# Performance work log

Measured on AMD Instinct MI355X. Metric: run time of the kernel, lower is better.

## Reference

```python
import jax, jax.numpy as jnp
import numpy as np

EMBED_DIM = 1024
NUM_HEADS = 16
HEAD_DIM = EMBED_DIM // NUM_HEADS


def setup_inputs() -> dict:
    key = jax.random.key(0)
    k1, k2, k3, k4, k5 = jax.random.split(key, 5)
    B, T, C = 4, 2048, EMBED_DIM
    scale = 1.0 / np.sqrt(C)
    return {
        "x": jax.random.normal(k1, (B, T, C), dtype=jnp.float32),
        "W_qkv": jax.random.normal(k2, (3 * C, C), dtype=jnp.float32) * scale,
        "b_qkv": jax.random.normal(k3, (3 * C,), dtype=jnp.float32) * 0.02,
        "W_proj": jax.random.normal(k4, (C, C), dtype=jnp.float32) * scale,
        "b_proj": jax.random.normal(k5, (C,), dtype=jnp.float32) * 0.02,
    }


def reference(x, W_qkv, b_qkv, W_proj, b_proj):
    B, T, C = x.shape
    H, D = NUM_HEADS, HEAD_DIM
    qkv = x @ W_qkv.T + b_qkv                      # [B,T,3C]
    q, k, v = jnp.split(qkv, 3, axis=-1)
    q = q.reshape(B, T, H, D).transpose(0, 2, 1, 3)  # [B,H,T,D]
    k = k.reshape(B, T, H, D).transpose(0, 2, 1, 3)
    v = v.reshape(B, T, H, D).transpose(0, 2, 1, 3)
    scores = jnp.einsum("bhqd,bhkd->bhqk", q, k) / np.sqrt(D)  # [B,H,T,T]
    causal = jnp.tril(jnp.ones((T, T), dtype=bool))
    scores = jnp.where(causal, scores, -jnp.inf)
    attn = jax.nn.softmax(scores, axis=-1)
    out = jnp.einsum("bhqk,bhkd->bhqd", attn, v)   # [B,H,T,D]
    out = out.transpose(0, 2, 1, 3).reshape(B, T, C)
    return out @ W_proj.T + b_proj
```

## Files before the change

### kernel.cpp

```cpp
#include <hip/hip_runtime.h>
#include <math.h>

#define EMBED 1024
#define NHEAD 16
#define HDIM  64
#define SEQT  2048
#define BATCH 4

typedef __bf16 bf16x4 __attribute__((ext_vector_type(4)));
typedef __bf16 bf16x8 __attribute__((ext_vector_type(8)));
typedef float  f32x4  __attribute__((ext_vector_type(4)));

#define AS1 __attribute__((address_space(1)))
#define AS3 __attribute__((address_space(3)))
#define GLD_LDS16(gp, lp) __builtin_amdgcn_global_load_lds( \
    (const AS1 unsigned int*)(gp), (AS3 unsigned int*)(lp), 16, 0, 0)

#define QSCALE 0.180336880f

__device__ __forceinline__ unsigned short f2bf_hw(float f) {
    union { __bf16 h; unsigned short u; } c; c.h = (__bf16)f; return c.u;
}

__global__ __launch_bounds__(256)
void cvt_all(const float* __restrict__ x, const float* __restrict__ wq,
             const float* __restrict__ wp,
             unsigned short* __restrict__ xb, unsigned short* __restrict__ wqb,
             unsigned short* __restrict__ wpb)
{
    const int N1 = 2097152;
    const int N2 = 786432;
    int i = blockIdx.x * 256 + threadIdx.x;
    const float4* src; ushort4* dst; int j;
    if (i < N1)            { src = (const float4*)x;  dst = (ushort4*)xb;  j = i; }
    else if (i < N1 + N2)  { src = (const float4*)wq; dst = (ushort4*)wqb; j = i - N1; }
    else                   { src = (const float4*)wp; dst = (ushort4*)wpb; j = i - N1 - N2; }
    float4 v = src[j];
    ushort4 o;
    o.x = f2bf_hw(v.x); o.y = f2bf_hw(v.y); o.z = f2bf_hw(v.z); o.w = f2bf_hw(v.w);
    dst[j] = o;
}

template<int MODE>
__global__ __launch_bounds__(256)
void gemm_bt_mfma(const unsigned short* __restrict__ A, const unsigned short* __restrict__ Bw,
                  const float* __restrict__ bias,
                  void* out0, void* out1, void* out2,
                  int M, int N, int K)
{
    __shared__ __align__(16) unsigned short Asm[2][128 * 32];
    __shared__ __align__(16) unsigned short Bsm[2][128 * 32];

    const int tid  = threadIdx.x;
    const int lane = tid & 63;
    const int wave = tid >> 6;
    const int wm = wave >> 1, wn = wave & 1;
    const int col = lane & 15, quad = lane >> 4;
    const long m0 = (long)blockIdx.y * 128, n0 = (long)blockIdx.x * 128;

    f32x4 acc[4][4];
#pragma unroll
    for (int mi = 0; mi < 4; mi++)
#pragma unroll
        for (int ni = 0; ni < 4; ni++) acc[mi][ni] = (f32x4){0.f, 0.f, 0.f, 0.f};

    const int lrow = tid >> 2;
    const int lcol = (tid & 3) * 8;
    const unsigned short* Ag = A + (m0 + lrow) * K + lcol;
    const unsigned short* Bg = Bw + (n0 + lrow) * K + lcol;

    GLD_LDS16(Ag,                &Asm[0][0] + tid * 8);
    GLD_LDS16(Ag + (long)64 * K, &Asm[0][0] + 2048 + tid * 8);
    GLD_LDS16(Bg,                &Bsm[0][0] + tid * 8);
    GLD_LDS16(Bg + (long)64 * K, &Bsm[0][0] + 2048 + tid * 8);

    const int iters = K >> 5;
    for (int it = 0; it < iters; it++) {
        const int cur = it & 1;
        __builtin_amdgcn_s_waitcnt(0x0F70);
        __syncthreads();
        if (it + 1 < iters) {
            const int kk = (it + 1) * 32, nxt = cur ^ 1;
            GLD_LDS16(Ag + kk,                &Asm[nxt][0] + tid * 8);
            GLD_LDS16(Ag + (long)64 * K + kk, &Asm[nxt][0] + 2048 + tid * 8);
            GLD_LDS16(Bg + kk,                &Bsm[nxt][0] + tid * 8);
            GLD_LDS16(Bg + (long)64 * K + kk, &Bsm[nxt][0] + 2048 + tid * 8);
        }

        bf16x8 af[4], bf[4];
#pragma unroll
        for (int mi = 0; mi < 4; mi++)
            af[mi] = *(const bf16x8*)&Asm[cur][(wm * 64 + mi * 16 + col) * 32 + quad * 8];
#pragma unroll
        for (int ni = 0; ni < 4; ni++)
            bf[ni] = *(const bf16x8*)&Bsm[cur][(wn * 64 + ni * 16 + col) * 32 + quad * 8];
#pragma unroll
        for (int mi = 0; mi < 4; mi++)
#pragma unroll
            for (int ni = 0; ni < 4; ni++)
                acc[mi][ni] = __builtin_amdgcn_mfma_f32_16x16x32_bf16(af[mi], bf[ni], acc[mi][ni], 0, 0, 0);
    }

#pragma unroll
    for (int mi = 0; mi < 4; mi++) {
#pragma unroll
        for (int ni = 0; ni < 4; ni++) {
            long n = n0 + wn * 64 + ni * 16 + col;
            float bv = bias[n];
#pragma unroll
            for (int r = 0; r < 4; r++) {
                long m = m0 + wm * 64 + mi * 16 + quad * 4 + r;
                float v = acc[mi][ni][r] + bv;
                if (MODE == 0) {
                    ((float*)out0)[m * N + n] = v;
                } else {
                    int which = (int)(n >> 10);
                    int c = (int)(n & 1023);
                    int h = c >> 6, d = c & 63;
                    int b = (int)(m >> 11), t = (int)(m & 2047);
                    long bh = (long)(b * NHEAD + h);
                    if (which == 0)      ((unsigned short*)out0)[(bh * SEQT + t) * HDIM + d] = f2bf_hw(v * QSCALE);
                    else if (which == 1) ((unsigned short*)out1)[(bh * SEQT + t) * HDIM + d] = f2bf_hw(v);
                    else                 ((unsigned short*)out2)[(bh * HDIM + d) * SEQT + t] = f2bf_hw(v);
                }
            }
        }
    }
}

#define PPAD 72

__global__ __launch_bounds__(256, 3)
void flash_attn_mfma4(const unsigned short* __restrict__ Qb,
                      const unsigned short* __restrict__ Kb,
                      const unsigned short* __restrict__ Vt,
                      unsigned short* __restrict__ Ob)
{
    __shared__ __align__(16) unsigned short P_lds[128 * PPAD];
    __shared__ __align__(16) unsigned short K_lds[2][64 * 64];
    __shared__ __align__(16) unsigned short V_lds[2][64 * 64];
    __shared__ __align__(16) float L_lds[128];

    const int tid  = threadIdx.x;
    const int lane = tid & 63;
    const int wave = tid >> 6;
    const int col  = lane & 15;
    const int quad = lane >> 4;

    const int idx = blockIdx.x;
    const int qt = 15 - (idx >> 6);
    const int hb = idx & 63;
    const int h = hb & 15, b = hb >> 4;
    const int q0 = qt * 128;
    const long bh = (long)(b * NHEAD + h);
    const unsigned short* Kbh = Kb + bh * SEQT * HDIM;
    const unsigned short* Vbh = Vt + bh * HDIM * SEQT;
    const int ktiles = 2 * qt + 2;

    const int r0 = tid >> 3,         c0 = (tid & 7) ^ (r0 & 7);
    const int r1 = (tid + 256) >> 3, c1 = (tid & 7) ^ (r1 & 7);

    bf16x8 qf[2][2];
#pragma unroll
    for (int ni = 0; ni < 2; ni++) {
        const unsigned short* qrow = Qb + (bh * SEQT + q0 + wave * 32 + ni * 16 + col) * HDIM;
        qf[ni][0] = *(const bf16x8*)(qrow + quad * 8);
        qf[ni][1] = *(const bf16x8*)(qrow + 32 + quad * 8);
    }

    GLD_LDS16(Kbh + r0 * HDIM + c0 * 8,        &K_lds[0][0] + tid * 8);
    GLD_LDS16(Kbh + r1 * HDIM + c1 * 8,        &K_lds[0][0] + 2048 + tid * 8);
    GLD_LDS16(Vbh + (long)r0 * SEQT + c0 * 8,  &V_lds[0][0] + tid * 8);
    GLD_LDS16(Vbh + (long)r1 * SEQT + c1 * 8,  &V_lds[0][0] + 2048 + tid * 8);

    f32x4 o[2][4];
#pragma unroll
    for (int mi = 0; mi < 2; mi++)
#pragma unroll
        for (int dt = 0; dt < 4; dt++) o[mi][dt] = (f32x4){0.f, 0.f, 0.f, 0.f};
    float rs[2] = {0.f, 0.f};

    const int cswz0 = quad ^ (col & 7);
    const int cswz1 = (quad + 4) ^ (col & 7);

    for (int kt = 0; kt < ktiles; kt++) {
        const int cur = kt & 1;
        __builtin_amdgcn_s_waitcnt(0x0F70);
        __syncthreads();
        if (kt + 1 < ktiles) {
            const int k0n = (kt + 1) * 64, nxt = cur ^ 1;
            GLD_LDS16(Kbh + (k0n + r0) * HDIM + c0 * 8,       &K_lds[nxt][0] + tid * 8);
            GLD_LDS16(Kbh + (k0n + r1) * HDIM + c1 * 8,       &K_lds[nxt][0] + 2048 + tid * 8);
            GLD_LDS16(Vbh + (long)r0 * SEQT + k0n + c0 * 8,   &V_lds[nxt][0] + tid * 8);
            GLD_LDS16(Vbh + (long)r1 * SEQT + k0n + c1 * 8,   &V_lds[nxt][0] + 2048 + tid * 8);
        }

        const unsigned short* Kc = &K_lds[cur][0];
        f32x4 st[4][2];
#pragma unroll
        for (int mt = 0; mt < 4; mt++) {
            const int row = mt * 16 + col;
            bf16x8 kf0 = *(const bf16x8*)&Kc[row * 64 + cswz0 * 8];
            bf16x8 kf1 = *(const bf16x8*)&Kc[row * 64 + cswz1 * 8];
#pragma unroll
            for (int ni = 0; ni < 2; ni++) {
                f32x4 acc = (f32x4){0.f, 0.f, 0.f, 0.f};
                acc = __builtin_amdgcn_mfma_f32_16x16x32_bf16(kf0, qf[ni][0], acc, 0, 0, 0);
                acc = __builtin_amdgcn_mfma_f32_16x16x32_bf16(kf1, qf[ni][1], acc, 0, 0, 0);
                st[mt][ni] = acc;
            }
        }
        const int k0 = kt * 64;
        if (kt >= 2 * qt) {
#pragma unroll
            for (int mt = 0; mt < 4; mt++) {
                const int keybase = k0 + mt * 16 + quad * 4;
#pragma unroll
                for (int ni = 0; ni < 2; ni++) {
                    const int qg = q0 + wave * 32 + ni * 16 + col;
#pragma unroll
                    for (int r = 0; r < 4; r++)
                        if (keybase + r > qg) st[mt][ni][r] = -INFINITY;
                }
            }
        }

#pragma unroll
        for (int mt = 0; mt < 4; mt++)
#pragma unroll
            for (int ni = 0; ni < 2; ni++) {
                f32x4 p;
#pragma unroll
                for (int r = 0; r < 4; r++) p[r] = __builtin_amdgcn_exp2f(st[mt][ni][r]);
                rs[ni] += (p[0] + p[1]) + (p[2] + p[3]);
                bf16x4 pb = __builtin_convertvector(p, bf16x4);
                *(bf16x4*)&P_lds[(wave * 32 + ni * 16 + col) * PPAD + mt * 16 + quad * 4] = pb;
            }

        const unsigned short* Vc = &V_lds[cur][0];
#pragma unroll
        for (int mi = 0; mi < 2; mi++) {
            const unsigned short* prow = &P_lds[(wave * 32 + mi * 16 + col) * PPAD];
            bf16x8 pf0 = *(const bf16x8*)(prow + quad * 8);
            bf16x8 pf1 = *(const bf16x8*)(prow + 32 + quad * 8);
#pragma unroll
            for (int dt = 0; dt < 4; dt++) {
                const int row = dt * 16 + col;
                bf16x8 vf0 = *(const bf16x8*)&Vc[row * 64 + cswz0 * 8];
                bf16x8 vf1 = *(const bf16x8*)&Vc[row * 64 + cswz1 * 8];
                o[mi][dt] = __builtin_amdgcn_mfma_f32_16x16x32_bf16(pf0, vf0, o[mi][dt], 0, 0, 0);
                o[mi][dt] = __builtin_amdgcn_mfma_f32_16x16x32_bf16(pf1, vf1, o[mi][dt], 0, 0, 0);
            }
        }
    }

#pragma unroll
    for (int ni = 0; ni < 2; ni++) {
        rs[ni] += __shfl_xor(rs[ni], 16);
        rs[ni] += __shfl_xor(rs[ni], 32);
        if (quad == 0) L_lds[wave * 32 + ni * 16 + col] = rs[ni];
    }
    f32x4 lf[2];
#pragma unroll
    for (int mi = 0; mi < 2; mi++)
        lf[mi] = *(const f32x4*)&L_lds[wave * 32 + mi * 16 + quad * 4];

#pragma unroll
    for (int mi = 0; mi < 2; mi++)
#pragma unroll
        for (int r = 0; r < 4; r++) {
            float inv = 1.f / lf[mi][r];
            int t = q0 + wave * 32 + mi * 16 + quad * 4 + r;
            unsigned short* orow = Ob + ((long)(b * SEQT + t)) * EMBED + h * HDIM;
#pragma unroll
            for (int dt = 0; dt < 4; dt++)
                orow[dt * 16 + col] = f2bf_hw(o[mi][dt][r] * inv);
        }
}

extern "C" void kernel_launch(void* const* d_in, const int* in_sizes, int n_in,
                              void* d_out, int out_size, void* d_ws, size_t ws_size,
                              hipStream_t stream)
{
    const float* x     = (const float*)d_in[0];
    const float* Wqkv  = (const float*)d_in[1];
    const float* bqkv  = (const float*)d_in[2];
    const float* Wproj = (const float*)d_in[3];
    const float* bproj = (const float*)d_in[4];
    float* out = (float*)d_out;

    const long Mbt = (long)BATCH * SEQT;
    const long per = (long)BATCH * NHEAD * SEQT * HDIM;

    unsigned short* xb  = (unsigned short*)d_ws;
    unsigned short* wqb = xb  + per;
    unsigned short* wpb = wqb + 3 * EMBED * EMBED;
    unsigned short* Qb  = wpb + EMBED * EMBED;
    unsigned short* Kb  = Qb + per;
    unsigned short* Vt  = Kb + per;
    unsigned short* Ob  = Vt + per;

    cvt_all<<<12288, 256, 0, stream>>>(x, Wqkv, Wproj, xb, wqb, wpb);

    dim3 g1(3 * EMBED / 128, Mbt / 128);
    gemm_bt_mfma<1><<<g1, 256, 0, stream>>>(xb, wqb, bqkv, Qb, Kb, Vt,
                                            (int)Mbt, 3 * EMBED, EMBED);

    flash_attn_mfma4<<<1024, 256, 0, stream>>>(Qb, Kb, Vt, Ob);

    dim3 g3(EMBED / 128, Mbt / 128);
    gemm_bt_mfma<0><<<g3, 256, 0, stream>>>(Ob, wpb, bproj, out, nullptr, nullptr,
                                            (int)Mbt, EMBED, EMBED);
}
```

Measured before the change: 258.6 us.

## Rewrite GEMMs as 256x256 tiles with swizzled LDS and phased MFMA schedule

Replaces the 128x128, 256-thread GEMM with a 256x256, 512-thread kernel that stages 64-wide K slices into XOR-swizzled LDS. Each iteration is split into barrier-separated phases that interleave LDS fragment loads with MFMA quadrants under raised wave priority. The goal is more operand reuse per load, fewer LDS bank conflicts, and overlap of global-to-LDS copies with compute. The trade-offs are 128KB of LDS per block and far fewer blocks: the projection GEMM gets only 128 blocks, which may underfill the GPU. It also adds a missing __syncthreads in the attention kernel before L_lds is read.

```diff
diff --git a/kernel.cpp b/kernel.cpp
--- a/kernel.cpp
+++ b/kernel.cpp
@@ -41,75 +41,114 @@
     dst[j] = o;
 }
 
+#define BAR do { __builtin_amdgcn_sched_barrier(0); \
+                 __builtin_amdgcn_s_barrier(); \
+                 __builtin_amdgcn_sched_barrier(0); } while (0)
+
 template<int MODE>
-__global__ __launch_bounds__(256)
-void gemm_bt_mfma(const unsigned short* __restrict__ A, const unsigned short* __restrict__ Bw,
-                  const float* __restrict__ bias,
-                  void* out0, void* out1, void* out2,
-                  int M, int N, int K)
+__global__ __launch_bounds__(512, 2)
+void gemm_bt_8ph(const unsigned short* __restrict__ A, const unsigned short* __restrict__ Bw,
+                 const float* __restrict__ bias,
+                 void* out0, void* out1, void* out2,
+                 int M, int N, int K)
 {
-    __shared__ __align__(16) unsigned short Asm[2][128 * 32];
-    __shared__ __align__(16) unsigned short Bsm[2][128 * 32];
+    __shared__ __align__(16) unsigned short Asm[2][256 * 64];
+    __shared__ __align__(16) unsigned short Bsm[2][256 * 64];
 
     const int tid  = threadIdx.x;
     const int lane = tid & 63;
     const int wave = tid >> 6;
-    const int wm = wave >> 1, wn = wave & 1;
+    const int wm = wave >> 2, wn = wave & 3;
     const int col = lane & 15, quad = lane >> 4;
-    const long m0 = (long)blockIdx.y * 128, n0 = (long)blockIdx.x * 128;
-
-    f32x4 acc[4][4];
-#pragma unroll
-    for (int mi = 0; mi < 4; mi++)
+    const long m0 = (long)blockIdx.y * 256, n0 = (long)blockIdx.x * 256;
+
+    f32x4 acc[8][4];
+#pragma unroll
+    for (int mi = 0; mi < 8; mi++)
 #pragma unroll
         for (int ni = 0; ni < 4; ni++) acc[mi][ni] = (f32x4){0.f, 0.f, 0.f, 0.f};
 
-    const int lrow = tid >> 2;
-    const int lcol = (tid & 3) * 8;
-    const unsigned short* Ag = A + (m0 + lrow) * K + lcol;
-    const unsigned short* Bg = Bw + (n0 + lrow) * K + lcol;
-
-    GLD_LDS16(Ag,                &Asm[0][0] + tid * 8);
-    GLD_LDS16(Ag + (long)64 * K, &Asm[0][0] + 2048 + tid * 8);
-    GLD_LDS16(Bg,                &Bsm[0][0] + tid * 8);
-    GLD_LDS16(Bg + (long)64 * K, &Bsm[0][0] + 2048 + tid * 8);
-
-    const int iters = K >> 5;
-    for (int it = 0; it < iters; it++) {
-        const int cur = it & 1;
+    const int srow  = tid >> 3;
+    const int sslot = tid & 7;
+    const int gslot = sslot ^ (srow & 7);
+    const unsigned short* Agb = A  + (m0 + srow) * (long)K + gslot * 8;
+    const unsigned short* Bgb = Bw + (n0 + srow) * (long)K + gslot * 8;
+
+#define STAGE(b, kt_) do { const long ko_ = (long)(kt_) * 64; \
+    _Pragma("unroll") for (int r_ = 0; r_ < 4; r_++) { \
+        GLD_LDS16(Agb + (long)r_ * 64 * K + ko_, &Asm[b][0] + r_ * 4096 + tid * 8); \
+        GLD_LDS16(Bgb + (long)r_ * 64 * K + ko_, &Bsm[b][0] + r_ * 4096 + tid * 8); \
+    } } while (0)
+
+#define LOAD_A(qm_) do { _Pragma("unroll") for (int i_ = 0; i_ < 4; i_++) { \
+        const int row_ = wm * 128 + ((qm_) * 4 + i_) * 16 + col; \
+        const int rx_ = row_ & 7; \
+        af[i_][0] = *(const bf16x8*)&Ac[row_ * 64 + ((quad    ) ^ rx_) * 8]; \
+        af[i_][1] = *(const bf16x8*)&Ac[row_ * 64 + ((quad + 4) ^ rx_) * 8]; \
+    } } while (0)
+
+#define LOAD_B(qn_) do { _Pragma("unroll") for (int j_ = 0; j_ < 2; j_++) { \
+        const int row_ = wn * 64 + ((qn_) * 2 + j_) * 16 + col; \
+        const int rx_ = row_ & 7; \
+        bfv[j_][0] = *(const bf16x8*)&Bc[row_ * 64 + ((quad    ) ^ rx_) * 8]; \
+        bfv[j_][1] = *(const bf16x8*)&Bc[row_ * 64 + ((quad + 4) ^ rx_) * 8]; \
+    } } while (0)
+
+#define MFMA_Q(qm_, qn_) do { __builtin_amdgcn_s_setprio(1); \
+    _Pragma("unroll") for (int i_ = 0; i_ < 4; i_++) \
+    _Pragma("unroll") for (int j_ = 0; j_ < 2; j_++) { \
+        acc[(qm_) * 4 + i_][(qn_) * 2 + j_] = __builtin_amdgcn_mfma_f32_16x16x32_bf16( \
+            af[i_][0], bfv[j_][0], acc[(qm_) * 4 + i_][(qn_) * 2 + j_], 0, 0, 0); \
+        acc[(qm_) * 4 + i_][(qn_) * 2 + j_] = __builtin_amdgcn_mfma_f32_16x16x32_bf16( \
+            af[i_][1], bfv[j_][1], acc[(qm_) * 4 + i_][(qn_) * 2 + j_], 0, 0, 0); \
+    } \
+    __builtin_amdgcn_s_setprio(0); } while (0)
+
+    STAGE(0, 0);
+    __builtin_amdgcn_s_waitcnt(0x0F70);
+    BAR;
+
+    const int T = K >> 6;
+    for (int kt = 0; kt < T; kt++) {
+        const int cur = kt & 1;
+        const unsigned short* Ac = &Asm[cur][0];
+        const unsigned short* Bc = &Bsm[cur][0];
+        bf16x8 af[4][2], bfv[2][2];
+
+        LOAD_A(0); LOAD_B(0);
+        if (kt + 1 < T) STAGE(cur ^ 1, kt + 1);
+        BAR;
+        MFMA_Q(0, 0);
+        BAR;
+        LOAD_B(1);
+        BAR;
+        MFMA_Q(0, 1);
+        BAR;
+        LOAD_A(1);
+        BAR;
+        MFMA_Q(1, 1);
+        BAR;
+        LOAD_B(0);
+        BAR;
+        MFMA_Q(1, 0);
         __builtin_amdgcn_s_waitcnt(0x0F70);
-        __syncthreads();
-        if (it + 1 < iters) {
-            const int kk = (it + 1) * 32, nxt = cur ^ 1;
-            GLD_LDS16(Ag + kk,                &Asm[nxt][0] + tid * 8);
-            GLD_LDS16(Ag + (long)64 * K + kk, &Asm[nxt][0] + 2048 + tid * 8);
-            GLD_LDS16(Bg + kk,                &Bsm[nxt][0] + tid * 8);
-            GLD_LDS16(Bg + (long)64 * K + kk, &Bsm[nxt][0] + 2048 + tid * 8);
-        }
-
-        bf16x8 af[4], bf[4];
-#pragma unroll
-        for (int mi = 0; mi < 4; mi++)
-            af[mi] = *(const bf16x8*)&Asm[cur][(wm * 64 + mi * 16 + col) * 32 + quad * 8];
-#pragma unroll
-        for (int ni = 0; ni < 4; ni++)
-            bf[ni] = *(const bf16x8*)&Bsm[cur][(wn * 64 + ni * 16 + col) * 32 + quad * 8];
-#pragma unroll
-        for (int mi = 0; mi < 4; mi++)
-#pragma unroll
-            for (int ni = 0; ni < 4; ni++)
-                acc[mi][ni] = __builtin_amdgcn_mfma_f32_16x16x32_bf16(af[mi], bf[ni], acc[mi][ni], 0, 0, 0);
-    }
-
-#pragma unroll
-    for (int mi = 0; mi < 4; mi++) {
+        BAR;
+    }
+
+#undef STAGE
+#undef LOAD_A
+#undef LOAD_B
+#undef MFMA_Q
+
+#pragma unroll
+    for (int mi = 0; mi < 8; mi++) {
 #pragma unroll
         for (int ni = 0; ni < 4; ni++) {
             long n = n0 + wn * 64 + ni * 16 + col;
             float bv = bias[n];
 #pragma unroll
             for (int r = 0; r < 4; r++) {
-                long m = m0 + wm * 64 + mi * 16 + quad * 4 + r;
+                long m = m0 + wm * 128 + mi * 16 + quad * 4 + r;
                 float v = acc[mi][ni][r] + bv;
                 if (MODE == 0) {
                     ((float*)out0)[m * N + n] = v;
@@ -260,6 +299,7 @@
         rs[ni] += __shfl_xor(rs[ni], 32);
         if (quad == 0) L_lds[wave * 32 + ni * 16 + col] = rs[ni];
     }
+    __syncthreads();
     f32x4 lf[2];
 #pragma unroll
     for (int mi = 0; mi < 2; mi++)
@@ -302,13 +342,13 @@
 
     cvt_all<<<12288, 256, 0, stream>>>(x, Wqkv, Wproj, xb, wqb, wpb);
 
-    dim3 g1(3 * EMBED / 128, Mbt / 128);
-    gemm_bt_mfma<1><<<g1, 256, 0, stream>>>(xb, wqb, bqkv, Qb, Kb, Vt,
-                                            (int)Mbt, 3 * EMBED, EMBED);
+    dim3 g1(3 * EMBED / 256, Mbt / 256);
+    gemm_bt_8ph<1><<<g1, 512, 0, stream>>>(xb, wqb, bqkv, Qb, Kb, Vt,
+                                           (int)Mbt, 3 * EMBED, EMBED);
 
     flash_attn_mfma4<<<1024, 256, 0, stream>>>(Qb, Kb, Vt, Ob);
 
-    dim3 g3(EMBED / 128, Mbt / 128);
-    gemm_bt_mfma<0><<<g3, 256, 0, stream>>>(Ob, wpb, bproj, out, nullptr, nullptr,
-                                            (int)Mbt, EMBED, EMBED);
-}
+    dim3 g3(EMBED / 256, Mbt / 256);
+    gemm_bt_8ph<0><<<g3, 512, 0, stream>>>(Ob, wpb, bproj, out, nullptr, nullptr,
+                                           (int)Mbt, EMBED, EMBED);
+}
```

Result: slower. 284.2 us (+9.9%).
